# Kernel tuning notes

Hardware: AMD Instinct MI355X
Metric: run time of the kernel (lower is better)

Reference implementation:

```python
import jax, jax.numpy as jnp
import numpy as np

N = 200000
D = 128
PARAM_SCALE = 1.0 / D  # keep exp() exponent bounded (original torch.rand init overflows at scale)


def setup_inputs() -> dict:
    key = jax.random.key(0)
    kx, k1, k2, k3, k4 = jax.random.split(key, 5)
    X = jax.random.normal(kx, (N, D), dtype=jnp.float32)
    W_sum = jax.random.uniform(k1, (D, D), dtype=jnp.float32) * PARAM_SCALE
    W_alpha = jax.random.uniform(k2, (D, D), dtype=jnp.float32) * PARAM_SCALE
    a_alpha = jax.random.uniform(k3, (D, 1), dtype=jnp.float32) * PARAM_SCALE
    b_alpha = jax.random.uniform(k4, (D, 1), dtype=jnp.float32) * PARAM_SCALE
    return {"X": X, "W_sum": W_sum, "W_alpha": W_alpha,
            "a_alpha": a_alpha, "b_alpha": b_alpha}


def reference(X, W_sum, W_alpha, a_alpha, b_alpha):
    # a_w = a_alpha^T @ W_alpha, b_w = b_alpha^T @ W_alpha  -> (D,) each
    a_w = a_alpha[:, 0] @ W_alpha
    b_w = b_alpha[:, 0] @ W_alpha
    # alpha_j = exp(a_w . X[0] + b_w . X[j])  -> (N,)
    alpha = jnp.exp(a_w @ X[0] + X @ b_w)
    # weighted sum over all rows, normalized by sum of (unnormalized) weights
    sum_output = (alpha @ X) / jnp.sum(alpha)  # (D,)
    return sum_output @ W_sum  # (D,)
```

## Files before the change

### kernel.cpp

```cpp
#include <hip/hip_runtime.h>
#include <hip/hip_bf16.h>

#define D 128


__global__ __launch_bounds__(1024) void prep_kernel(
    const float* __restrict__ W_alpha,
    const float* __restrict__ b_alpha,
    float* __restrict__ bw_out)
{
    const int t = threadIdx.x;
    const int k = t & 127;
    const int g = t >> 7;
    __shared__ float bal[D];
    if (t < D) bal[t] = b_alpha[t];
    __syncthreads();

    float bw = 0.f;
    #pragma unroll
    for (int i = g * 16; i < g * 16 + 16; ++i)
        bw = fmaf(bal[i], W_alpha[i * D + k], bw);

    __shared__ float rbw[8][D];
    rbw[g][k] = bw;
    __syncthreads();
    if (t < D) {
        float B = 0.f;
        #pragma unroll
        for (int r = 0; r < 8; ++r) B += rbw[r][t];
        bw_out[t] = B;
    }
}

__global__ __launch_bounds__(256, 8) void main_pass_kernel(
    const float* __restrict__ X,
    const float* __restrict__ bw,
    float* __restrict__ partial_wsum,
    float* __restrict__ partial_alpha,
    int nrows)
{
    const int t    = threadIdx.x;
    const int col4 = t & 31;
    const int rg   = t >> 5;

    const float4 bwv = reinterpret_cast<const float4*>(bw)[col4];

    float a0 = 0.f, a1 = 0.f, a2 = 0.f, a3 = 0.f;
    float aacc = 0.f;

    const int ftiles = nrows >> 4;
    const float4* __restrict__ X4 = reinterpret_cast<const float4*>(X);

    int tile = blockIdx.x;
    size_t addr = ((size_t)blockIdx.x * 16 + rg * 2) * 32 + col4;
    const size_t step = (size_t)gridDim.x * 512;

    float4 x0, x1;
    if (tile < ftiles) { x0 = X4[addr]; x1 = X4[addr + 32]; }

    while (tile < ftiles) {
        const int ntile = tile + gridDim.x;
        const size_t naddr = addr + (ntile < ftiles ? step : (size_t)0);
        const float4 n0 = X4[naddr];
        const float4 n1 = X4[naddr + 32];

        float d0 = fmaf(x0.x, bwv.x, fmaf(x0.y, bwv.y, fmaf(x0.z, bwv.z, x0.w * bwv.w)));
        float d1 = fmaf(x1.x, bwv.x, fmaf(x1.y, bwv.y, fmaf(x1.z, bwv.z, x1.w * bwv.w)));
        #pragma unroll
        for (int m = 16; m >= 1; m >>= 1) {
            d0 += __shfl_xor(d0, m, 64);
            d1 += __shfl_xor(d1, m, 64);
        }
        const float al0 = __expf(d0);
        const float al1 = __expf(d1);
        aacc += al0 + al1;
        a0 = fmaf(al0, x0.x, fmaf(al1, x1.x, a0));
        a1 = fmaf(al0, x0.y, fmaf(al1, x1.y, a1));
        a2 = fmaf(al0, x0.z, fmaf(al1, x1.z, a2));
        a3 = fmaf(al0, x0.w, fmaf(al1, x1.w, a3));

        x0 = n0; x1 = n1; addr = naddr; tile = ntile;
    }

    const int rem = nrows & 15;
    if (rem && blockIdx.x == 0) {
        const int r0 = (nrows & ~15) + rg * 2;
        if (r0 < nrows) {
            const float4 x0r = X4[(size_t)r0 * 32 + col4];
            const bool v1 = (r0 + 1) < nrows;
            const float4 x1r = v1 ? X4[(size_t)(r0 + 1) * 32 + col4]
                                  : make_float4(0.f, 0.f, 0.f, 0.f);
            float d0 = fmaf(x0r.x, bwv.x, fmaf(x0r.y, bwv.y, fmaf(x0r.z, bwv.z, x0r.w * bwv.w)));
            float d1 = fmaf(x1r.x, bwv.x, fmaf(x1r.y, bwv.y, fmaf(x1r.z, bwv.z, x1r.w * bwv.w)));
            #pragma unroll
            for (int m = 16; m >= 1; m >>= 1) {
                d0 += __shfl_xor(d0, m, 64);
                d1 += __shfl_xor(d1, m, 64);
            }
            const float al0 = __expf(d0);
            const float al1 = v1 ? __expf(d1) : 0.f;
            aacc += al0 + al1;
            a0 = fmaf(al0, x0r.x, fmaf(al1, x1r.x, a0));
            a1 = fmaf(al0, x0r.y, fmaf(al1, x1r.y, a1));
            a2 = fmaf(al0, x0r.z, fmaf(al1, x1r.z, a2));
            a3 = fmaf(al0, x0r.w, fmaf(al1, x1r.w, a3));
        }
    }

    __shared__ float red[8][32][4];
    __shared__ float reda[8];
    red[rg][col4][0] = a0;
    red[rg][col4][1] = a1;
    red[rg][col4][2] = a2;
    red[rg][col4][3] = a3;
    if (col4 == 0) reda[rg] = aacc;
    __syncthreads();

    if (t < D) {
        double s = 0.0;
        #pragma unroll
        for (int r = 0; r < 8; ++r) s += (double)red[r][t >> 2][t & 3];
        partial_wsum[(size_t)blockIdx.x * D + t] = (float)s;
    }
    if (t == 0) {
        double s = 0.0;
        #pragma unroll
        for (int r = 0; r < 8; ++r) s += (double)reda[r];
        partial_alpha[blockIdx.x] = (float)s;
    }
}

__global__ __launch_bounds__(512) void reduce1_kernel(
    const float* __restrict__ partial_wsum,
    const float* __restrict__ partial_alpha,
    float* __restrict__ mid,
    float* __restrict__ mida,
    int NB, int NB2)
{
    const int b  = blockIdx.x;
    const int t  = threadIdx.x;
    const int k  = t & 127;
    const int rs = t >> 7;
    const int nper = NB / NB2;

    double s = 0.0;
    for (int j = rs; j < nper; j += 4)
        s += (double)partial_wsum[(size_t)(b + NB2 * j) * D + k];
    __shared__ double red[4][D];
    red[rs][k] = s;

    __shared__ double reda[64];
    if (t < 64) {
        double sa = 0.0;
        for (int j = t; j < nper; j += 64) sa += (double)partial_alpha[b + NB2 * j];
        reda[t] = sa;
    }
    __syncthreads();

    if (t < D)
        mid[(size_t)b * D + t] = (float)(red[0][t] + red[1][t] + red[2][t] + red[3][t]);
    if (t == 0) {
        double sa = 0.0;
        const int lim = nper < 64 ? nper : 64;
        for (int i = 0; i < lim; ++i) sa += reda[i];
        mida[b] = (float)sa;
    }
}

__global__ __launch_bounds__(1024) void final_kernel(
    const float* __restrict__ mid,
    const float* __restrict__ mida,
    const float* __restrict__ W_sum,
    float* __restrict__ out,
    int NB2)
{
    const int t = threadIdx.x;
    const int k = t & 127;
    const int g = t >> 7;

    const float4* __restrict__ W4 = reinterpret_cast<const float4*>(W_sum);
    float4 w0 = W4[t], w1 = W4[t + 1024], w2 = W4[t + 2048], w3 = W4[t + 3072];

    __shared__ float red[8][D];
    float ws = 0.f;
    #pragma unroll
    for (int j = 0; j < 8; ++j) {
        const int row = g + j * 8;
        if (row < NB2) ws += mid[(size_t)row * D + k];
    }
    red[g][k] = ws;

    __shared__ float reda[64];
    if (t < 64) reda[t] = (t < NB2) ? mida[t] : 0.f;

    __shared__ float wls[D * D];
    float4* wls4 = reinterpret_cast<float4*>(wls);
    wls4[t] = w0; wls4[t + 1024] = w1; wls4[t + 2048] = w2; wls4[t + 3072] = w3;
    __syncthreads();

    __shared__ double asum_sh;
    if (t == 0) {
        double a = 0.0;
        #pragma unroll
        for (int i = 0; i < 64; ++i) a += (double)reda[i];
        asum_sh = a;
    }
    __syncthreads();

    __shared__ float s_sh[D];
    if (t < D) {
        double s = 0.0;
        #pragma unroll
        for (int r = 0; r < 8; ++r) s += (double)red[r][t];
        s_sh[t] = (float)(s / asum_sh);
    }
    __syncthreads();

    float o = 0.f;
    #pragma unroll
    for (int kk = g * 16; kk < g * 16 + 16; ++kk)
        o = fmaf(s_sh[kk], wls[kk * D + k], o);
    __shared__ float rout[8][D];
    rout[g][k] = o;
    __syncthreads();
    if (t < D) {
        float s = 0.f;
        #pragma unroll
        for (int r = 0; r < 8; ++r) s += rout[r][t];
        out[t] = s;
    }
}

extern "C" void kernel_launch(void* const* d_in, const int* in_sizes, int n_in,
                              void* d_out, int out_size, void* d_ws, size_t ws_size,
                              hipStream_t stream) {
    const float* X       = (const float*)d_in[0];
    const float* W_sum   = (const float*)d_in[1];
    const float* W_alpha = (const float*)d_in[2];
    const float* b_alpha = (const float*)d_in[4];
    float* out = (float*)d_out;

    const int nrows = in_sizes[0] / D;
    const int NB2 = 64;

    int NB = 2048;
    auto need = [&](int nb) {
        return (size_t)nb * (D + 1) * sizeof(float)
             + 256
             + (size_t)NB2 * (D + 1) * sizeof(float)
             + (D + 8) * sizeof(float);
    };
    while (NB > NB2 && need(NB) > ws_size) NB >>= 1;

    char* ws = (char*)d_ws;
    float* partial_wsum  = (float*)ws;
    float* partial_alpha = (float*)(ws + (size_t)NB * D * sizeof(float));
    size_t off = (size_t)NB * (D + 1) * sizeof(float);
    off = (off + 255) & ~(size_t)255;
    float* mid  = (float*)(ws + off);
    float* mida = mid + (size_t)NB2 * D;
    float* bw   = mida + NB2;

    prep_kernel<<<1, 1024, 0, stream>>>(W_alpha, b_alpha, bw);
    main_pass_kernel<<<NB, 256, 0, stream>>>(X, bw, partial_wsum,
                                             partial_alpha, nrows);
    reduce1_kernel<<<NB2, 512, 0, stream>>>(partial_wsum, partial_alpha,
                                            mid, mida, NB, NB2);
    final_kernel<<<1, 1024, 0, stream>>>(mid, mida, W_sum, out, NB2);
}
```

Baseline: 36.44 us.

## Deepen X prefetch to two tiles and merge reduction kernels into one final pass

The main pass now keeps two tiles of X in flight (a distance-2 software prefetch) instead of one, to hide more global-memory latency. The grid shrinks from 2048 to 1024 blocks, and the two-stage reduction (reduce1 plus final) becomes a single final kernel that sums all block partials directly, removing one launch. Per-block partial sums use float instead of double. The trade-off is fewer blocks to saturate bandwidth, more registers per thread, and a longer serial reduction in a single block.

```diff
diff --git a/kernel.cpp b/kernel.cpp
--- a/kernel.cpp
+++ b/kernel.cpp
@@ -50,36 +50,44 @@
 
     const int ftiles = nrows >> 4;
     const float4* __restrict__ X4 = reinterpret_cast<const float4*>(X);
+    const int    gstep = gridDim.x;
+    const size_t step  = (size_t)gstep * 512;
 
     int tile = blockIdx.x;
-    size_t addr = ((size_t)blockIdx.x * 16 + rg * 2) * 32 + col4;
-    const size_t step = (size_t)gridDim.x * 512;
-
-    float4 x0, x1;
-    if (tile < ftiles) { x0 = X4[addr]; x1 = X4[addr + 32]; }
-
-    while (tile < ftiles) {
-        const int ntile = tile + gridDim.x;
-        const size_t naddr = addr + (ntile < ftiles ? step : (size_t)0);
-        const float4 n0 = X4[naddr];
-        const float4 n1 = X4[naddr + 32];
-
-        float d0 = fmaf(x0.x, bwv.x, fmaf(x0.y, bwv.y, fmaf(x0.z, bwv.z, x0.w * bwv.w)));
-        float d1 = fmaf(x1.x, bwv.x, fmaf(x1.y, bwv.y, fmaf(x1.z, bwv.z, x1.w * bwv.w)));
-        #pragma unroll
-        for (int m = 16; m >= 1; m >>= 1) {
-            d0 += __shfl_xor(d0, m, 64);
-            d1 += __shfl_xor(d1, m, 64);
+
+    if (tile < ftiles) {
+        size_t addr0 = ((size_t)tile * 16 + rg * 2) * 32 + col4;
+        float4 x0 = X4[addr0];
+        float4 x1 = X4[addr0 + 32];
+        size_t addr1 = addr0 + ((tile + gstep < ftiles) ? step : (size_t)0);
+        float4 n0 = X4[addr1];
+        float4 n1 = X4[addr1 + 32];
+
+        while (tile < ftiles) {
+            const size_t addr2 =
+                addr1 + ((tile + 2 * gstep < ftiles) ? step : (size_t)0);
+            const float4 p0 = X4[addr2];
+            const float4 p1 = X4[addr2 + 32];
+
+            float d0 = fmaf(x0.x, bwv.x, fmaf(x0.y, bwv.y, fmaf(x0.z, bwv.z, x0.w * bwv.w)));
+            float d1 = fmaf(x1.x, bwv.x, fmaf(x1.y, bwv.y, fmaf(x1.z, bwv.z, x1.w * bwv.w)));
+            #pragma unroll
+            for (int m = 16; m >= 1; m >>= 1) {
+                d0 += __shfl_xor(d0, m, 64);
+                d1 += __shfl_xor(d1, m, 64);
+            }
+            const float al0 = __expf(d0);
+            const float al1 = __expf(d1);
+            aacc += al0 + al1;
+            a0 = fmaf(al0, x0.x, fmaf(al1, x1.x, a0));
+            a1 = fmaf(al0, x0.y, fmaf(al1, x1.y, a1));
+            a2 = fmaf(al0, x0.z, fmaf(al1, x1.z, a2));
+            a3 = fmaf(al0, x0.w, fmaf(al1, x1.w, a3));
+
+            x0 = n0; x1 = n1; n0 = p0; n1 = p1;
+            addr1 = addr2;
+            tile += gstep;
         }
-        const float al0 = __expf(d0);
-        const float al1 = __expf(d1);
-        aacc += al0 + al1;
-        a0 = fmaf(al0, x0.x, fmaf(al1, x1.x, a0));
-        a1 = fmaf(al0, x0.y, fmaf(al1, x1.y, a1));
-        a2 = fmaf(al0, x0.z, fmaf(al1, x1.z, a2));
-        a3 = fmaf(al0, x0.w, fmaf(al1, x1.w, a3));
-
-        x0 = n0; x1 = n1; addr = naddr; tile = ntile;
     }
 
     const int rem = nrows & 15;
@@ -117,62 +125,25 @@
     __syncthreads();
 
     if (t < D) {
-        double s = 0.0;
-        #pragma unroll
-        for (int r = 0; r < 8; ++r) s += (double)red[r][t >> 2][t & 3];
-        partial_wsum[(size_t)blockIdx.x * D + t] = (float)s;
+        float s = 0.f;
+        #pragma unroll
+        for (int r = 0; r < 8; ++r) s += red[r][t >> 2][t & 3];
+        partial_wsum[(size_t)blockIdx.x * D + t] = s;
     }
     if (t == 0) {
-        double s = 0.0;
-        #pragma unroll
-        for (int r = 0; r < 8; ++r) s += (double)reda[r];
-        partial_alpha[blockIdx.x] = (float)s;
-    }
-}
-
-__global__ __launch_bounds__(512) void reduce1_kernel(
+        float s = 0.f;
+        #pragma unroll
+        for (int r = 0; r < 8; ++r) s += reda[r];
+        partial_alpha[blockIdx.x] = s;
+    }
+}
+
+__global__ __launch_bounds__(1024) void final2_kernel(
     const float* __restrict__ partial_wsum,
     const float* __restrict__ partial_alpha,
-    float* __restrict__ mid,
-    float* __restrict__ mida,
-    int NB, int NB2)
-{
-    const int b  = blockIdx.x;
-    const int t  = threadIdx.x;
-    const int k  = t & 127;
-    const int rs = t >> 7;
-    const int nper = NB / NB2;
-
-    double s = 0.0;
-    for (int j = rs; j < nper; j += 4)
-        s += (double)partial_wsum[(size_t)(b + NB2 * j) * D + k];
-    __shared__ double red[4][D];
-    red[rs][k] = s;
-
-    __shared__ double reda[64];
-    if (t < 64) {
-        double sa = 0.0;
-        for (int j = t; j < nper; j += 64) sa += (double)partial_alpha[b + NB2 * j];
-        reda[t] = sa;
-    }
-    __syncthreads();
-
-    if (t < D)
-        mid[(size_t)b * D + t] = (float)(red[0][t] + red[1][t] + red[2][t] + red[3][t]);
-    if (t == 0) {
-        double sa = 0.0;
-        const int lim = nper < 64 ? nper : 64;
-        for (int i = 0; i < lim; ++i) sa += reda[i];
-        mida[b] = (float)sa;
-    }
-}
-
-__global__ __launch_bounds__(1024) void final_kernel(
-    const float* __restrict__ mid,
-    const float* __restrict__ mida,
     const float* __restrict__ W_sum,
     float* __restrict__ out,
-    int NB2)
+    int NB)
 {
     const int t = threadIdx.x;
     const int k = t & 127;
@@ -181,38 +152,35 @@
     const float4* __restrict__ W4 = reinterpret_cast<const float4*>(W_sum);
     float4 w0 = W4[t], w1 = W4[t + 1024], w2 = W4[t + 2048], w3 = W4[t + 3072];
 
-    __shared__ float red[8][D];
-    float ws = 0.f;
-    #pragma unroll
-    for (int j = 0; j < 8; ++j) {
-        const int row = g + j * 8;
-        if (row < NB2) ws += mid[(size_t)row * D + k];
-    }
+    double ap = (t < NB) ? (double)partial_alpha[t] : 0.0;
+
+    double ws = 0.0;
+    for (int r = g; r < NB; r += 8)
+        ws += (double)partial_wsum[(size_t)r * D + k];
+    __shared__ double red[8][D];
     red[g][k] = ws;
 
-    __shared__ float reda[64];
-    if (t < 64) reda[t] = (t < NB2) ? mida[t] : 0.f;
+    __shared__ double reda[1024];
+    reda[t] = ap;
 
     __shared__ float wls[D * D];
     float4* wls4 = reinterpret_cast<float4*>(wls);
     wls4[t] = w0; wls4[t + 1024] = w1; wls4[t + 2048] = w2; wls4[t + 3072] = w3;
     __syncthreads();
 
-    __shared__ double asum_sh;
-    if (t == 0) {
-        double a = 0.0;
-        #pragma unroll
-        for (int i = 0; i < 64; ++i) a += (double)reda[i];
-        asum_sh = a;
-    }
-    __syncthreads();
+    #pragma unroll
+    for (int s = 512; s >= 1; s >>= 1) {
+        if (t < s) reda[t] += reda[t + s];
+        __syncthreads();
+    }
+    const double asum = reda[0];
 
     __shared__ float s_sh[D];
     if (t < D) {
         double s = 0.0;
         #pragma unroll
-        for (int r = 0; r < 8; ++r) s += (double)red[r][t];
-        s_sh[t] = (float)(s / asum_sh);
+        for (int r = 0; r < 8; ++r) s += red[r][t];
+        s_sh[t] = (float)(s / asum);
     }
     __syncthreads();
 
@@ -241,30 +209,24 @@
     float* out = (float*)d_out;
 
     const int nrows = in_sizes[0] / D;
-    const int NB2 = 64;
-
-    int NB = 2048;
+
+    int NB = 1024;
     auto need = [&](int nb) {
         return (size_t)nb * (D + 1) * sizeof(float)
-             + 256
-             + (size_t)NB2 * (D + 1) * sizeof(float)
-             + (D + 8) * sizeof(float);
+             + 256 + (D + 8) * sizeof(float);
     };
-    while (NB > NB2 && need(NB) > ws_size) NB >>= 1;
+    while (NB > 64 && need(NB) > ws_size) NB >>= 1;
 
     char* ws = (char*)d_ws;
     float* partial_wsum  = (float*)ws;
     float* partial_alpha = (float*)(ws + (size_t)NB * D * sizeof(float));
     size_t off = (size_t)NB * (D + 1) * sizeof(float);
     off = (off + 255) & ~(size_t)255;
-    float* mid  = (float*)(ws + off);
-    float* mida = mid + (size_t)NB2 * D;
-    float* bw   = mida + NB2;
+    float* bw = (float*)(ws + off);
 
     prep_kernel<<<1, 1024, 0, stream>>>(W_alpha, b_alpha, bw);
     main_pass_kernel<<<NB, 256, 0, stream>>>(X, bw, partial_wsum,
                                              partial_alpha, nrows);
-    reduce1_kernel<<<NB2, 512, 0, stream>>>(partial_wsum, partial_alpha,
-                                            mid, mida, NB, NB2);
-    final_kernel<<<1, 1024, 0, stream>>>(mid, mida, W_sum, out, NB2);
-}
+    final2_kernel<<<1, 1024, 0, stream>>>(partial_wsum, partial_alpha,
+                                          W_sum, out, NB);
+}
```

Result: slower. 64.87 us (+78.0%).
